# Kernel optimization log

Hardware: AMD Instinct MI355X
Metric: run time of the kernel (lower is better)

The kernel has to match this reference:

```python
import jax, jax.numpy as jnp
import numpy as np

N = 8192
E = 262144
D_IN = 512
H1 = 32
H2 = 16
EPS = 1e-32


def setup_inputs() -> dict:
    key = jax.random.key(0)
    ks = jax.random.split(key, 7)
    X = jax.random.normal(ks[0], (N, D_IN), dtype=jnp.float32)
    edge_row = jax.random.randint(ks[1], (E,), 0, N, dtype=jnp.int64 if jax.config.read('jax_enable_x64') else jnp.int32).astype(jnp.int32)
    edge_col = jax.random.randint(ks[2], (E,), 0, N, dtype=jnp.int32)
    edge_val = jax.random.uniform(ks[3], (E,), dtype=jnp.float32)
    # glorot-style init scale (uniform in [-r, r])
    def glorot(k, din, dout):
        r = np.sqrt(6.0 / (din + dout)).astype(np.float32)
        return jax.random.uniform(k, (din, dout), dtype=jnp.float32, minval=-r, maxval=r)
    W0 = glorot(ks[4], D_IN, H1)
    W1 = glorot(ks[5], H1, H2)
    W2 = glorot(ks[6], H1, H2)
    return {"X": X, "edge_row": edge_row, "edge_col": edge_col,
            "edge_val": edge_val, "W0": W0, "W1": W1, "W2": W2}


def _spmm(edge_row, edge_col, edge_val, x):
    # out[i] = sum_j adj[i, j] * x[j] over COO edges
    gathered = edge_val[:, None] * x[edge_col]  # [E, d]
    return jax.ops.segment_sum(gathered, edge_row, num_segments=N)


def reference(X, edge_row, edge_col, edge_val, W0, W1, W2):
    # GraphConvSparse: adj @ (X @ W) then activation
    hidden = jax.nn.relu(_spmm(edge_row, edge_col, edge_val, X @ W0))      # [N, H1]
    mean = _spmm(edge_row, edge_col, edge_val, hidden @ W1)                 # [N, H2]
    std = _spmm(edge_row, edge_col, edge_val, hidden @ W2)                  # [N, H2]
    mean = jnp.maximum(mean, EPS)  # mean[mean < 1e-32] = 1e-32
    std = jnp.maximum(std, EPS)    # kept for parity; unused in eval path
    Z = mean  # eval mode: sampled_z = mean
    A_pred = jax.nn.sigmoid(Z @ Z.T)  # [N, N] dot-product decode
    return A_pred
```

## Files before the change

### kernel.cpp

```cpp
#include <hip/hip_runtime.h>

#define NN   8192
#define DIN  512
#define H1   32
#define H2   16
#define NE   262144
#define EPSV 1e-32f

__global__ __launch_bounds__(256) void k_xw0(const float* __restrict__ X,
                                             const float* __restrict__ W0,
                                             float* __restrict__ XW0) {
    int t = blockIdx.x * 256 + threadIdx.x;
    int r = t >> 5, c = t & 31;
    const float4* Xr = reinterpret_cast<const float4*>(X + (size_t)r * DIN);
    float acc = 0.f;
#pragma unroll 8
    for (int k4 = 0; k4 < DIN / 4; ++k4) {
        float4 x = Xr[k4];
        int k = k4 * 4;
        acc = fmaf(x.x, W0[(k + 0) * H1 + c], acc);
        acc = fmaf(x.y, W0[(k + 1) * H1 + c], acc);
        acc = fmaf(x.z, W0[(k + 2) * H1 + c], acc);
        acc = fmaf(x.w, W0[(k + 3) * H1 + c], acc);
    }
    XW0[t] = acc;
}

__global__ __launch_bounds__(256) void k_spmm1(const int* __restrict__ er,
                                               const int* __restrict__ ec,
                                               const float* __restrict__ ev,
                                               const float* __restrict__ XW0,
                                               float* __restrict__ hacc) {
    int t = blockIdx.x * 256 + threadIdx.x;
    int e = t >> 5, c = t & 31;
    int row = er[e], col = ec[e];
    float v = ev[e];
    atomicAdd(&hacc[row * H1 + c], v * XW0[col * H1 + c]);
}

__global__ __launch_bounds__(256) void k_hw1(const float* __restrict__ hacc,
                                             const float* __restrict__ W1,
                                             float* __restrict__ HW1) {
    int t = blockIdx.x * 256 + threadIdx.x;
    int r = t >> 4, c = t & 15;
    const float* hr = hacc + r * H1;
    float acc = 0.f;
#pragma unroll
    for (int k = 0; k < H1; ++k)
        acc = fmaf(fmaxf(hr[k], 0.f), W1[k * H2 + c], acc);
    HW1[t] = acc;
}

__global__ __launch_bounds__(256) void k_spmm2(const int* __restrict__ er,
                                               const int* __restrict__ ec,
                                               const float* __restrict__ ev,
                                               const float* __restrict__ HW1,
                                               float* __restrict__ mean) {
    int t = blockIdx.x * 256 + threadIdx.x;
    int e = t >> 4, c = t & 15;
    int row = er[e], col = ec[e];
    float v = ev[e];
    atomicAdd(&mean[row * H2 + c], v * HW1[col * H2 + c]);
}

#define TI  128
#define PAD 20

__device__ __forceinline__ float sigm(float x) {
    return __fdividef(1.0f, 1.0f + __expf(-x));
}

__global__ __launch_bounds__(256) void k_decode(const float* __restrict__ Zm,
                                                float* __restrict__ out) {
    __shared__ float zi[TI * PAD];
    __shared__ float zj[TI * PAD];
    const int i0 = blockIdx.y * TI, j0 = blockIdx.x * TI;
    const int tid = threadIdx.x;

#pragma unroll
    for (int l = 0; l < 2; ++l) {
        int t = tid + l * 256;
        int r = t >> 2, c4 = (t & 3) * 4;
        float4 a = *reinterpret_cast<const float4*>(Zm + (size_t)(i0 + r) * H2 + c4);
        float4 b = *reinterpret_cast<const float4*>(Zm + (size_t)(j0 + r) * H2 + c4);
        a.x = fmaxf(a.x, EPSV); a.y = fmaxf(a.y, EPSV);
        a.z = fmaxf(a.z, EPSV); a.w = fmaxf(a.w, EPSV);
        b.x = fmaxf(b.x, EPSV); b.y = fmaxf(b.y, EPSV);
        b.z = fmaxf(b.z, EPSV); b.w = fmaxf(b.w, EPSV);
        *reinterpret_cast<float4*>(&zi[r * PAD + c4]) = a;
        *reinterpret_cast<float4*>(&zj[r * PAD + c4]) = b;
    }
    __syncthreads();

    const int tx = tid & 15, ty = tid >> 4;
    float acc[8][8] = {};
#pragma unroll
    for (int k4 = 0; k4 < 4; ++k4) {
        float4 ra[8], rb[8];
#pragma unroll
        for (int a = 0; a < 8; ++a)
            ra[a] = *reinterpret_cast<const float4*>(&zi[(ty * 8 + a) * PAD + k4 * 4]);
#pragma unroll
        for (int b = 0; b < 8; ++b)
            rb[b] = *reinterpret_cast<const float4*>(&zj[(tx * 8 + b) * PAD + k4 * 4]);
#pragma unroll
        for (int a = 0; a < 8; ++a)
#pragma unroll
            for (int b = 0; b < 8; ++b) {
                acc[a][b] = fmaf(ra[a].x, rb[b].x, acc[a][b]);
                acc[a][b] = fmaf(ra[a].y, rb[b].y, acc[a][b]);
                acc[a][b] = fmaf(ra[a].z, rb[b].z, acc[a][b]);
                acc[a][b] = fmaf(ra[a].w, rb[b].w, acc[a][b]);
            }
    }

#pragma unroll
    for (int a = 0; a < 8; ++a) {
        size_t rowbase = (size_t)(i0 + ty * 8 + a) * NN + j0 + tx * 8;
#pragma unroll
        for (int b4 = 0; b4 < 8; b4 += 4) {
            float4 o;
            o.x = sigm(acc[a][b4 + 0]);
            o.y = sigm(acc[a][b4 + 1]);
            o.z = sigm(acc[a][b4 + 2]);
            o.w = sigm(acc[a][b4 + 3]);
            *reinterpret_cast<float4*>(out + rowbase + b4) = o;
        }
    }
}

extern "C" void kernel_launch(void* const* d_in, const int* in_sizes, int n_in,
                              void* d_out, int out_size, void* d_ws, size_t ws_size,
                              hipStream_t stream) {
    const float* X  = (const float*)d_in[0];
    const int*   er = (const int*)d_in[1];
    const int*   ec = (const int*)d_in[2];
    const float* ev = (const float*)d_in[3];
    const float* W0 = (const float*)d_in[4];
    const float* W1 = (const float*)d_in[5];
    float* out = (float*)d_out;

    char* ws = (char*)d_ws;
    float* XW0  = (float*)(ws);
    float* hacc = (float*)(ws + (1 << 20));
    float* mean = (float*)(ws + (2 << 20));
    float* HW1  = (float*)(ws + (2 << 20) + (512 << 10));

    hipMemsetAsync(hacc, 0, (1 << 20) + (512 << 10), stream);

    k_xw0  <<<NN * H1 / 256, 256, 0, stream>>>(X, W0, XW0);
    k_spmm1<<<NE * H1 / 256, 256, 0, stream>>>(er, ec, ev, XW0, hacc);
    k_hw1  <<<NN * H2 / 256, 256, 0, stream>>>(hacc, W1, HW1);
    k_spmm2<<<NE * H2 / 256, 256, 0, stream>>>(er, ec, ev, HW1, mean);
    k_decode<<<dim3(NN / TI, NN / TI), 256, 0, stream>>>(mean, out);
}
```

Baseline: 380.9 us.

## Convert COO edges to CSR on device and use atomic-free row-wise SpMM

Builds a CSR representation each call with a histogram, single-block scan and atomic scatter, then runs both SpMMs as per-row gathers with two accumulators. This replaces the per-edge float atomics into the hidden and mean buffers with plain stores. In exchange it adds three small kernels, each with integer atomics or a serial scan. Summation order within a row is now nondeterministic because the scatter order depends on atomics.

After: 390.8 us. +2.6%, slower.

```diff
diff --git a/kernel.cpp b/kernel.cpp
--- a/kernel.cpp
+++ b/kernel.cpp
@@ -26,16 +26,65 @@
     XW0[t] = acc;
 }
 
-__global__ __launch_bounds__(256) void k_spmm1(const int* __restrict__ er,
-                                               const int* __restrict__ ec,
-                                               const float* __restrict__ ev,
+__global__ __launch_bounds__(256) void k_hist(const int* __restrict__ er,
+                                              int* __restrict__ cnt) {
+    int e = blockIdx.x * 256 + threadIdx.x;
+    atomicAdd(&cnt[er[e]], 1);
+}
+
+__global__ __launch_bounds__(1024) void k_scan(const int* __restrict__ cnt,
+                                               int* __restrict__ rptr,
+                                               int* __restrict__ rfill) {
+    __shared__ int part[1024];
+    int tid = threadIdx.x;
+    int local[8];
+    int s = 0;
+#pragma unroll
+    for (int i = 0; i < 8; ++i) { local[i] = s; s += cnt[tid * 8 + i]; }
+    part[tid] = s;
+    __syncthreads();
+    for (int off = 1; off < 1024; off <<= 1) {
+        int v = (tid >= off) ? part[tid - off] : 0;
+        __syncthreads();
+        part[tid] += v;
+        __syncthreads();
+    }
+    int base = (tid == 0) ? 0 : part[tid - 1];
+#pragma unroll
+    for (int i = 0; i < 8; ++i) {
+        rptr[tid * 8 + i]  = base + local[i];
+        rfill[tid * 8 + i] = base + local[i];
+    }
+    if (tid == 1023) rptr[8192] = part[1023];
+}
+
+__global__ __launch_bounds__(256) void k_scatter(const int* __restrict__ er,
+                                                 const int* __restrict__ ec,
+                                                 const float* __restrict__ ev,
+                                                 int* __restrict__ rfill,
+                                                 int* __restrict__ ccol,
+                                                 float* __restrict__ cval) {
+    int e = blockIdx.x * 256 + threadIdx.x;
+    int p = atomicAdd(&rfill[er[e]], 1);
+    ccol[p] = ec[e];
+    cval[p] = ev[e];
+}
+
+__global__ __launch_bounds__(256) void k_spmm1(const int* __restrict__ rptr,
+                                               const int* __restrict__ ccol,
+                                               const float* __restrict__ cval,
                                                const float* __restrict__ XW0,
                                                float* __restrict__ hacc) {
     int t = blockIdx.x * 256 + threadIdx.x;
-    int e = t >> 5, c = t & 31;
-    int row = er[e], col = ec[e];
-    float v = ev[e];
-    atomicAdd(&hacc[row * H1 + c], v * XW0[col * H1 + c]);
+    int r = t >> 5, c = t & 31;
+    int p = rptr[r], end = rptr[r + 1];
+    float a0 = 0.f, a1 = 0.f;
+    for (; p + 2 <= end; p += 2) {
+        a0 = fmaf(cval[p],     XW0[ccol[p]     * H1 + c], a0);
+        a1 = fmaf(cval[p + 1], XW0[ccol[p + 1] * H1 + c], a1);
+    }
+    if (p < end) a0 = fmaf(cval[p], XW0[ccol[p] * H1 + c], a0);
+    hacc[t] = a0 + a1;
 }
 
 __global__ __launch_bounds__(256) void k_hw1(const float* __restrict__ hacc,
@@ -51,16 +100,21 @@
     HW1[t] = acc;
 }
 
-__global__ __launch_bounds__(256) void k_spmm2(const int* __restrict__ er,
-                                               const int* __restrict__ ec,
-                                               const float* __restrict__ ev,
+__global__ __launch_bounds__(256) void k_spmm2(const int* __restrict__ rptr,
+                                               const int* __restrict__ ccol,
+                                               const float* __restrict__ cval,
                                                const float* __restrict__ HW1,
                                                float* __restrict__ mean) {
     int t = blockIdx.x * 256 + threadIdx.x;
-    int e = t >> 4, c = t & 15;
-    int row = er[e], col = ec[e];
-    float v = ev[e];
-    atomicAdd(&mean[row * H2 + c], v * HW1[col * H2 + c]);
+    int r = t >> 4, c = t & 15;
+    int p = rptr[r], end = rptr[r + 1];
+    float a0 = 0.f, a1 = 0.f;
+    for (; p + 2 <= end; p += 2) {
+        a0 = fmaf(cval[p],     HW1[ccol[p]     * H2 + c], a0);
+        a1 = fmaf(cval[p + 1], HW1[ccol[p + 1] * H2 + c], a1);
+    }
+    if (p < end) a0 = fmaf(cval[p], HW1[ccol[p] * H2 + c], a0);
+    mean[t] = a0 + a1;
 }
 
 #define TI  128
@@ -145,12 +199,20 @@
     float* hacc = (float*)(ws + (1 << 20));
     float* mean = (float*)(ws + (2 << 20));
     float* HW1  = (float*)(ws + (2 << 20) + (512 << 10));
-
-    hipMemsetAsync(hacc, 0, (1 << 20) + (512 << 10), stream);
-
-    k_xw0  <<<NN * H1 / 256, 256, 0, stream>>>(X, W0, XW0);
-    k_spmm1<<<NE * H1 / 256, 256, 0, stream>>>(er, ec, ev, XW0, hacc);
-    k_hw1  <<<NN * H2 / 256, 256, 0, stream>>>(hacc, W1, HW1);
-    k_spmm2<<<NE * H2 / 256, 256, 0, stream>>>(er, ec, ev, HW1, mean);
-    k_decode<<<dim3(NN / TI, NN / TI), 256, 0, stream>>>(mean, out);
-}
+    int*   cnt  = (int*)  (ws + (3 << 20));
+    int*   rptr = (int*)  (ws + (3 << 20) + (64 << 10));
+    int*   rfill= (int*)  (ws + (3 << 20) + (128 << 10));
+    int*   ccol = (int*)  (ws + (3 << 20) + (192 << 10));
+    float* cval = (float*)(ws + (4 << 20) + (192 << 10));
+
+    hipMemsetAsync(cnt, 0, 32 << 10, stream);
+
+    k_xw0    <<<NN * H1 / 256, 256, 0, stream>>>(X, W0, XW0);
+    k_hist   <<<NE / 256, 256, 0, stream>>>(er, cnt);
+    k_scan   <<<1, 1024, 0, stream>>>(cnt, rptr, rfill);
+    k_scatter<<<NE / 256, 256, 0, stream>>>(er, ec, ev, rfill, ccol, cval);
+    k_spmm1  <<<NN * H1 / 256, 256, 0, stream>>>(rptr, ccol, cval, XW0, hacc);
+    k_hw1    <<<NN * H2 / 256, 256, 0, stream>>>(hacc, W1, HW1);
+    k_spmm2  <<<NN * H2 / 256, 256, 0, stream>>>(rptr, ccol, cval, HW1, mean);
+    k_decode <<<dim3(NN / TI, NN / TI), 256, 0, stream>>>(mean, out);
+}
```
